# Kernel optimization log

Hardware: AMD Instinct MI355X
Metric: run time of the kernel (lower is better)

## Reference

```python
import jax, jax.numpy as jnp
import numpy as np

GAMMA = 1.05  # VoxelSampler.GAMMA


def setup_inputs() -> dict:
    key = jax.random.key(0)
    k1, k2, k3, k4, k5 = jax.random.split(key, 5)
    B, T, R, Np, F = 2, 8, 128, 32768, 5
    # point xy within pc_range, remaining features (z, intensity, ...) gaussian
    xy = jax.random.uniform(k1, (B, T, Np, 2), minval=-75.0, maxval=75.0)
    rest = jax.random.normal(k2, (B, T, Np, F - 2))
    points = jnp.concatenate([xy, rest], axis=-1)  # [B,T,Np,5]
    # rois: [cx,cy,cz, dx,dy,dz, yaw, vx,vy]
    ctr = jax.random.uniform(k3, (B, T, R, 3), minval=-75.0, maxval=75.0)
    dims = jax.random.uniform(k4, (B, T, R, 3), minval=1.0, maxval=6.0)
    yaw_vel = jax.random.normal(k5, (B, T, R, 3))
    trajectory_rois = jnp.concatenate([ctr, dims, yaw_vel], axis=-1)  # [B,T,R,9]
    return {"points": points, "trajectory_rois": trajectory_rois, "num_sample": 32}


def reference(points, trajectory_rois, num_sample):
    # points: [B,T,Np,5] (pre-partitioned per batch/frame, mirrors the
    # batch-column + timestamp masking of the torch code with static shapes)
    # trajectory_rois: [B,T,R,9]
    B, T, R, _ = trajectory_rois.shape
    Fdim = points.shape[-1]
    # speed = ||roi[..., -2:]||, per-roi gamma = clamp((1.05*(1+speed))**(t/5), max=2.5)
    speed = jnp.linalg.norm(trajectory_rois[..., 7:9], axis=-1)          # [B,T,R]
    t_idx = jnp.arange(T, dtype=points.dtype)
    gamma = jnp.minimum((GAMMA * (1.0 + speed)) ** (t_idx[None, :, None] / 5.0), 2.5)
    # cylindrical radius per roi: ||dims_xy/2|| * gamma
    radiis = jnp.linalg.norm(trajectory_rois[..., 3:5] * 0.5, axis=-1) * gamma  # [B,T,R]
    cx = trajectory_rois[..., 0]
    cy = trajectory_rois[..., 1]
    px = points[..., 0]
    py = points[..., 1]
    dx = px[:, :, None, :] - cx[..., None]   # [B,T,R,Np]
    dy = py[:, :, None, :] - cy[..., None]
    dis = jnp.sqrt(dx * dx + dy * dy)        # [B,T,R,Np]
    in_radius = (dis <= radiis[..., None]).astype(points.dtype)
    # topk over 0/1 mask: picks num_sample in-radius points (lowest indices first),
    # exactly like torch.topk(point_mask.float(), num_sample)
    vals, idx = jax.lax.top_k(in_radius, num_sample)  # [B,T,R,S]
    sampled = jnp.take_along_axis(points[:, :, None, :, :], idx[..., None], axis=3)  # [B,T,R,S,5]
    sampled = jnp.where(vals[..., None] > 0, sampled, jnp.zeros((), dtype=points.dtype))
    # stack frames -> permute(0,2,1,3,4) -> flatten(2,3): [B,R,T*S,5]
    out = jnp.transpose(sampled, (0, 2, 1, 3, 4)).reshape(B, R, T * num_sample, Fdim)
    return out
```

## Files before the change

### kernel.cpp

```cpp
#include <hip/hip_runtime.h>
#include <math.h>

#define B_   2
#define T_   8
#define R_   128
#define NP_  32768
#define F_   5
#define S_   32
#define SEG_ 2048
#define NSEG (NP_ / SEG_)
#define NBT  (B_ * T_)
#define NROW (NBT * R_)
#define RPB  8

__device__ __forceinline__ int mbcnt64(unsigned long long m) {
    return __builtin_amdgcn_mbcnt_hi((unsigned)(m >> 32),
           __builtin_amdgcn_mbcnt_lo((unsigned)m, 0u));
}

__global__ __launch_bounds__(256) void xy_transpose_prep(
    const float* __restrict__ points,
    const float* __restrict__ rois,
    float2* __restrict__ xy,
    float4* __restrict__ rowc)
{
    const int j = blockIdx.x * blockDim.x + threadIdx.x;
    if (j < NBT * NP_ / 4) {
        const float4* src = (const float4*)points + (size_t)j * 5;
        const float4 a = src[0], b = src[1], c = src[2], d = src[3], e = src[4];
        float4* dst = (float4*)xy + (size_t)j * 2;
        dst[0] = make_float4(a.x, a.y, b.y, b.z);
        dst[1] = make_float4(c.z, c.w, d.w, e.x);
    }
    if (j < NROW) {
        const int row = j;
        const int bt  = row / R_;
        const int t   = bt % T_;
        const float* roi = rois + (size_t)row * 9;
        const float cx = roi[0], cy = roi[1];
        const float hx = roi[3] * 0.5f, hy = roi[4] * 0.5f;
        const float vx = roi[7], vy = roi[8];
        const float speed  = sqrtf(vx * vx + vy * vy);
        const float base_g = 1.05f * (1.0f + speed);
        const float expo   = (float)t / 5.0f;
        const float gamma  = fminf((float)pow((double)base_g, (double)expo), 2.5f);
        const float radius = sqrtf(hx * hx + hy * hy) * gamma;
        unsigned ut = __float_as_uint(radius * radius);
        while (sqrtf(__uint_as_float(ut)) > radius) --ut;
        while (sqrtf(__uint_as_float(ut + 1u)) <= radius) ++ut;
        rowc[row] = make_float4(cx, cy, __uint_as_float(ut), 0.0f);
    }
}

__global__ __launch_bounds__(256) void phase1_collect(
    const float2* __restrict__ xy,
    const float4* __restrict__ rowc,
    int* __restrict__ counts,
    unsigned short* __restrict__ hitidx)
{
    __shared__ float4 tile[SEG_ / 2];

    const int blk = blockIdx.x;
    const int rg  = blk % (R_ / RPB);
    const int bs  = blk / (R_ / RPB);
    const int seg = bs % NSEG;
    const int bt  = bs / NSEG;
    const int w    = threadIdx.x >> 6;
    const int lane = threadIdx.x & 63;

    const float4* src = (const float4*)(xy + (size_t)bt * NP_ + (size_t)seg * SEG_);
    #pragma unroll
    for (int i = 0; i < 4; ++i)
        tile[i * 256 + threadIdx.x] = src[i * 256 + threadIdx.x];
    __syncthreads();

    const int row0 = bt * R_ + rg * RPB + w * 2;
    const int row1 = row0 + 1;
    const float4 rc0 = rowc[row0], rc1 = rowc[row1];
    unsigned short* h0 = hitidx + ((size_t)row0 * NSEG + seg) * S_;
    unsigned short* h1 = hitidx + ((size_t)row1 * NSEG + seg) * S_;

    int sel0 = 0, sel1 = 0;
    const int ibase = seg * SEG_;
    #pragma unroll 2
    for (int it = 0; it < SEG_ / 128; ++it) {
        const float4 q = tile[it * 64 + lane];
        const int idx0 = ibase + (it * 64 + lane) * 2;

        {
            const float ax = __fsub_rn(q.x, rc0.x), ay = __fsub_rn(q.y, rc0.y);
            const float bx = __fsub_rn(q.z, rc0.x), by = __fsub_rn(q.w, rc0.y);
            const float d2a = __fadd_rn(__fmul_rn(ax, ax), __fmul_rn(ay, ay));
            const float d2b = __fadd_rn(__fmul_rn(bx, bx), __fmul_rn(by, by));
            const bool p0 = (d2a <= rc0.z), p1 = (d2b <= rc0.z);
            const unsigned long long m0 = __ballot(p0), m1 = __ballot(p1);
            if (m0 | m1) {
                const int base = sel0 + mbcnt64(m0) + mbcnt64(m1);
                if (p0 && base < S_) h0[base] = (unsigned short)idx0;
                if (p1) { const int s = base + (p0 ? 1 : 0);
                          if (s < S_) h0[s] = (unsigned short)(idx0 + 1); }
                sel0 += __popcll(m0) + __popcll(m1);
            }
        }
        {
            const float ax = __fsub_rn(q.x, rc1.x), ay = __fsub_rn(q.y, rc1.y);
            const float bx = __fsub_rn(q.z, rc1.x), by = __fsub_rn(q.w, rc1.y);
            const float d2a = __fadd_rn(__fmul_rn(ax, ax), __fmul_rn(ay, ay));
            const float d2b = __fadd_rn(__fmul_rn(bx, bx), __fmul_rn(by, by));
            const bool p0 = (d2a <= rc1.z), p1 = (d2b <= rc1.z);
            const unsigned long long m0 = __ballot(p0), m1 = __ballot(p1);
            if (m0 | m1) {
                const int base = sel1 + mbcnt64(m0) + mbcnt64(m1);
                if (p0 && base < S_) h1[base] = (unsigned short)idx0;
                if (p1) { const int s = base + (p0 ? 1 : 0);
                          if (s < S_) h1[s] = (unsigned short)(idx0 + 1); }
                sel1 += __popcll(m0) + __popcll(m1);
            }
        }
    }
    if (lane == 0) {
        counts[(size_t)row0 * NSEG + seg] = (sel0 < S_) ? sel0 : S_;
        counts[(size_t)row1 * NSEG + seg] = (sel1 < S_) ? sel1 : S_;
    }
}

__global__ __launch_bounds__(256) void phase2_gather(
    const float* __restrict__ points,
    const int* __restrict__ counts,
    const unsigned short* __restrict__ hitidx,
    float* __restrict__ out)
{
    const int tid  = blockIdx.x * blockDim.x + threadIdx.x;
    const int slot = tid & (S_ - 1);
    const int row  = tid >> 5;
    if (row >= NROW) return;
    const int r  = row % R_;
    const int bt = row / R_;
    const int t  = bt % T_;
    const int b  = bt / T_;

    const int4* cp = (const int4*)(counts + (size_t)row * NSEG);
    const int4 q0 = cp[0], q1 = cp[1], q2 = cp[2], q3 = cp[3];
    const int cs[16] = {q0.x,q0.y,q0.z,q0.w, q1.x,q1.y,q1.z,q1.w,
                        q2.x,q2.y,q2.z,q2.w, q3.x,q3.y,q3.z,q3.w};
    int seg = -1, local = 0, acc = 0;
    #pragma unroll
    for (int s = 0; s < NSEG; ++s) {
        const int na = acc + cs[s];
        if (seg < 0 && slot < na) { seg = s; local = slot - acc; }
        acc = na;
    }
    const int total = (acc < S_) ? acc : S_;

    float* o = out + (((((size_t)b * R_ + r) * T_ + t) * S_) + slot) * F_;
    if (slot < total) {
        const int pi = hitidx[((size_t)row * NSEG + seg) * S_ + local];
        const float* p = points + ((size_t)bt * NP_ + pi) * F_;
        o[0] = p[0]; o[1] = p[1]; o[2] = p[2]; o[3] = p[3]; o[4] = p[4];
    } else {
        o[0] = 0.0f; o[1] = 0.0f; o[2] = 0.0f; o[3] = 0.0f; o[4] = 0.0f;
    }
}

extern "C" void kernel_launch(void* const* d_in, const int* in_sizes, int n_in,
                              void* d_out, int out_size, void* d_ws, size_t ws_size,
                              hipStream_t stream) {
    const float* points = (const float*)d_in[0];
    const float* rois   = (const float*)d_in[1];
    float* out = (float*)d_out;

    char* ws = (char*)d_ws;
    float2* xy             = (float2*)ws;
    int* counts            = (int*)(ws + 4194304);
    unsigned short* hitidx = (unsigned short*)(ws + 4194304 + 131072);
    float4* rowc           = (float4*)(ws + 4194304 + 131072 + 2097152);

    xy_transpose_prep<<<(NBT * NP_ / 4 + 255) / 256, 256, 0, stream>>>(points, rois, xy, rowc);

    phase1_collect<<<NBT * NSEG * (R_ / RPB), 256, 0, stream>>>(xy, rowc, counts, hitidx);

    phase2_gather<<<(NROW * S_) / 256, 256, 0, stream>>>(points, counts, hitidx, out);
}
```

Measured before the change: 85.01 us.

## Fuse segmented scan and gather into one per-row streaming kernel with early exit

Replaces the segmented collect kernel and the separate gather kernel with one kernel. In it, each wavefront streams the whole point array for two ROI rows straight from global memory with register prefetch, keeps the first 32 hit indices in shared memory, and then writes the gathered output. It stops scanning once both rows have 32 hits, and it drops the global counts and hit-index buffers along with one launch. In exchange the grid shrinks to 256 blocks with fully serial scans per row, so parallelism and latency hiding drop sharply for rows that never fill.

```diff
diff --git a/kernel.cpp b/kernel.cpp
--- a/kernel.cpp
+++ b/kernel.cpp
@@ -7,11 +7,8 @@
 #define NP_  32768
 #define F_   5
 #define S_   32
-#define SEG_ 2048
-#define NSEG (NP_ / SEG_)
 #define NBT  (B_ * T_)
 #define NROW (NBT * R_)
-#define RPB  8
 
 __device__ __forceinline__ int mbcnt64(unsigned long long m) {
     return __builtin_amdgcn_mbcnt_hi((unsigned)(m >> 32),
@@ -52,109 +49,83 @@
     }
 }
 
-__global__ __launch_bounds__(256) void phase1_collect(
+
+#define PROC(qq, kk)                                                              \
+    {                                                                             \
+        const int idx0 = (it * 256 + (kk) * 64 + lane) * 2;                       \
+        {     \
+            const float ax = __fsub_rn(qq.x, rc0.x), ay = __fsub_rn(qq.y, rc0.y); \
+            const float bx = __fsub_rn(qq.z, rc0.x), by = __fsub_rn(qq.w, rc0.y); \
+            const float d2a = __fadd_rn(__fmul_rn(ax, ax), __fmul_rn(ay, ay));    \
+            const float d2b = __fadd_rn(__fmul_rn(bx, bx), __fmul_rn(by, by));    \
+            const bool p0 = (d2a <= rc0.z), p1 = (d2b <= rc0.z);                  \
+            const unsigned long long m0 = __ballot(p0), m1 = __ballot(p1);        \
+            if (m0 | m1) {                                                        \
+                const int base = sel0 + mbcnt64(m0) + mbcnt64(m1);                \
+                if (p0 && base < S_) hitbuf[w][0][base] = (unsigned short)idx0;   \
+                if (p1) { const int s2 = base + (p0 ? 1 : 0);                     \
+                          if (s2 < S_) hitbuf[w][0][s2] = (unsigned short)(idx0 + 1); } \
+                sel0 += __popcll(m0) + __popcll(m1);                              \
+            }                                                                     \
+        }                                                                         \
+        {                             \
+            const float ax = __fsub_rn(qq.x, rc1.x), ay = __fsub_rn(qq.y, rc1.y); \
+            const float bx = __fsub_rn(qq.z, rc1.x), by = __fsub_rn(qq.w, rc1.y); \
+            const float d2a = __fadd_rn(__fmul_rn(ax, ax), __fmul_rn(ay, ay));    \
+            const float d2b = __fadd_rn(__fmul_rn(bx, bx), __fmul_rn(by, by));    \
+            const bool p0 = (d2a <= rc1.z), p1 = (d2b <= rc1.z);                  \
+            const unsigned long long m0 = __ballot(p0), m1 = __ballot(p1);        \
+            if (m0 | m1) {                                                        \
+                const int base = sel1 + mbcnt64(m0) + mbcnt64(m1);                \
+                if (p0 && base < S_) hitbuf[w][1][base] = (unsigned short)idx0;   \
+                if (p1) { const int s2 = base + (p0 ? 1 : 0);                     \
+                          if (s2 < S_) hitbuf[w][1][s2] = (unsigned short)(idx0 + 1); } \
+                sel1 += __popcll(m0) + __popcll(m1);                              \
+            }                                                                     \
+        }                                                                         \
+    }
+
+__global__ __launch_bounds__(256) void fused_scan_emit(
     const float2* __restrict__ xy,
     const float4* __restrict__ rowc,
-    int* __restrict__ counts,
-    unsigned short* __restrict__ hitidx)
+    const float* __restrict__ points,
+    float* __restrict__ out)
 {
-    __shared__ float4 tile[SEG_ / 2];
-
-    const int blk = blockIdx.x;
-    const int rg  = blk % (R_ / RPB);
-    const int bs  = blk / (R_ / RPB);
-    const int seg = bs % NSEG;
-    const int bt  = bs / NSEG;
+    __shared__ unsigned short hitbuf[4][2][S_];
     const int w    = threadIdx.x >> 6;
     const int lane = threadIdx.x & 63;
+    const int row0 = blockIdx.x * 8 + w * 2;
+    const int row1 = row0 + 1;
+    const int bt   = row0 / R_;
+    const float4 rc0 = rowc[row0], rc1 = rowc[row1];
 
-    const float4* src = (const float4*)(xy + (size_t)bt * NP_ + (size_t)seg * SEG_);
-    #pragma unroll
-    for (int i = 0; i < 4; ++i)
-        tile[i * 256 + threadIdx.x] = src[i * 256 + threadIdx.x];
+    const float4* src = (const float4*)(xy + (size_t)bt * NP_) + lane;
+    int sel0 = 0, sel1 = 0;
+    float4 q0 = src[0], q1 = src[64], q2 = src[128], q3 = src[192];
+    src += 256;
+    int it = 0;
+    for (; it < 63; ++it) {
+        const float4 t0 = src[0], t1 = src[64], t2 = src[128], t3 = src[192];
+        src += 256;
+        PROC(q0, 0) PROC(q1, 1) PROC(q2, 2) PROC(q3, 3)
+        q0 = t0; q1 = t1; q2 = t2; q3 = t3;
+        if (sel0 >= S_ && sel1 >= S_) break;
+    }
+    if (it == 63) { PROC(q0, 0) PROC(q1, 1) PROC(q2, 2) PROC(q3, 3) }
+
     __syncthreads();
 
-    const int row0 = bt * R_ + rg * RPB + w * 2;
-    const int row1 = row0 + 1;
-    const float4 rc0 = rowc[row0], rc1 = rowc[row1];
-    unsigned short* h0 = hitidx + ((size_t)row0 * NSEG + seg) * S_;
-    unsigned short* h1 = hitidx + ((size_t)row1 * NSEG + seg) * S_;
-
-    int sel0 = 0, sel1 = 0;
-    const int ibase = seg * SEG_;
-    #pragma unroll 2
-    for (int it = 0; it < SEG_ / 128; ++it) {
-        const float4 q = tile[it * 64 + lane];
-        const int idx0 = ibase + (it * 64 + lane) * 2;
-
-        {
-            const float ax = __fsub_rn(q.x, rc0.x), ay = __fsub_rn(q.y, rc0.y);
-            const float bx = __fsub_rn(q.z, rc0.x), by = __fsub_rn(q.w, rc0.y);
-            const float d2a = __fadd_rn(__fmul_rn(ax, ax), __fmul_rn(ay, ay));
-            const float d2b = __fadd_rn(__fmul_rn(bx, bx), __fmul_rn(by, by));
-            const bool p0 = (d2a <= rc0.z), p1 = (d2b <= rc0.z);
-            const unsigned long long m0 = __ballot(p0), m1 = __ballot(p1);
-            if (m0 | m1) {
-                const int base = sel0 + mbcnt64(m0) + mbcnt64(m1);
-                if (p0 && base < S_) h0[base] = (unsigned short)idx0;
-                if (p1) { const int s = base + (p0 ? 1 : 0);
-                          if (s < S_) h0[s] = (unsigned short)(idx0 + 1); }
-                sel0 += __popcll(m0) + __popcll(m1);
-            }
-        }
-        {
-            const float ax = __fsub_rn(q.x, rc1.x), ay = __fsub_rn(q.y, rc1.y);
-            const float bx = __fsub_rn(q.z, rc1.x), by = __fsub_rn(q.w, rc1.y);
-            const float d2a = __fadd_rn(__fmul_rn(ax, ax), __fmul_rn(ay, ay));
-            const float d2b = __fadd_rn(__fmul_rn(bx, bx), __fmul_rn(by, by));
-            const bool p0 = (d2a <= rc1.z), p1 = (d2b <= rc1.z);
-            const unsigned long long m0 = __ballot(p0), m1 = __ballot(p1);
-            if (m0 | m1) {
-                const int base = sel1 + mbcnt64(m0) + mbcnt64(m1);
-                if (p0 && base < S_) h1[base] = (unsigned short)idx0;
-                if (p1) { const int s = base + (p0 ? 1 : 0);
-                          if (s < S_) h1[s] = (unsigned short)(idx0 + 1); }
-                sel1 += __popcll(m0) + __popcll(m1);
-            }
-        }
-    }
-    if (lane == 0) {
-        counts[(size_t)row0 * NSEG + seg] = (sel0 < S_) ? sel0 : S_;
-        counts[(size_t)row1 * NSEG + seg] = (sel1 < S_) ? sel1 : S_;
-    }
-}
-
-__global__ __launch_bounds__(256) void phase2_gather(
-    const float* __restrict__ points,
-    const int* __restrict__ counts,
-    const unsigned short* __restrict__ hitidx,
-    float* __restrict__ out)
-{
-    const int tid  = blockIdx.x * blockDim.x + threadIdx.x;
-    const int slot = tid & (S_ - 1);
-    const int row  = tid >> 5;
-    if (row >= NROW) return;
-    const int r  = row % R_;
-    const int bt = row / R_;
-    const int t  = bt % T_;
-    const int b  = bt / T_;
-
-    const int4* cp = (const int4*)(counts + (size_t)row * NSEG);
-    const int4 q0 = cp[0], q1 = cp[1], q2 = cp[2], q3 = cp[3];
-    const int cs[16] = {q0.x,q0.y,q0.z,q0.w, q1.x,q1.y,q1.z,q1.w,
-                        q2.x,q2.y,q2.z,q2.w, q3.x,q3.y,q3.z,q3.w};
-    int seg = -1, local = 0, acc = 0;
-    #pragma unroll
-    for (int s = 0; s < NSEG; ++s) {
-        const int na = acc + cs[s];
-        if (seg < 0 && slot < na) { seg = s; local = slot - acc; }
-        acc = na;
-    }
-    const int total = (acc < S_) ? acc : S_;
-
-    float* o = out + (((((size_t)b * R_ + r) * T_ + t) * S_) + slot) * F_;
-    if (slot < total) {
-        const int pi = hitidx[((size_t)row * NSEG + seg) * S_ + local];
+    const int half  = lane >> 5;
+    const int s     = lane & 31;
+    const int row   = half ? row1 : row0;
+    const int sel   = half ? sel1 : sel0;
+    const int total = sel < S_ ? sel : S_;
+    const int r = row % R_;
+    const int t = bt % T_;
+    const int b = bt / T_;
+    float* o = out + ((((size_t)b * R_ + r) * T_ + t) * S_ + s) * (size_t)F_;
+    if (s < total) {
+        const int pi = hitbuf[w][half][s];
         const float* p = points + ((size_t)bt * NP_ + pi) * F_;
         o[0] = p[0]; o[1] = p[1]; o[2] = p[2]; o[3] = p[3]; o[4] = p[4];
     } else {
@@ -170,14 +141,10 @@
     float* out = (float*)d_out;
 
     char* ws = (char*)d_ws;
-    float2* xy             = (float2*)ws;
-    int* counts            = (int*)(ws + 4194304);
-    unsigned short* hitidx = (unsigned short*)(ws + 4194304 + 131072);
-    float4* rowc           = (float4*)(ws + 4194304 + 131072 + 2097152);
+    float2* xy   = (float2*)ws;
+    float4* rowc = (float4*)(ws + 4194304);
 
     xy_transpose_prep<<<(NBT * NP_ / 4 + 255) / 256, 256, 0, stream>>>(points, rois, xy, rowc);
 
-    phase1_collect<<<NBT * NSEG * (R_ / RPB), 256, 0, stream>>>(xy, rowc, counts, hitidx);
-
-    phase2_gather<<<(NROW * S_) / 256, 256, 0, stream>>>(points, counts, hitidx, out);
+    fused_scan_emit<<<NROW / 8, 256, 0, stream>>>(xy, rowc, points, out);
 }
```

Result: slower. 107.5 us (+26.4%).
